# Performance work log

Measured on AMD Instinct MI355X. Metric: run time of the kernel, lower is better.

Reference implementation:

```python
import jax, jax.numpy as jnp
import numpy as np

B, T, N, D, H, M = 2, 12, 325, 64, 8, 3
EPS = 1e-6


def _layer_norm(x, g, b):
    mu = jnp.mean(x, axis=-1, keepdims=True)
    var = jnp.mean(jnp.square(x - mu), axis=-1, keepdims=True)
    return (x - mu) * jax.lax.rsqrt(var + EPS) * g + b


def _meta_w(ste, W1, b1, W2, b2):
    # ste: (b,t,n,d) -> per-token weight matrix (b,t,n,d,d)  [Meta_projection]
    h = jax.nn.relu(jnp.einsum('btnd,de->btne', ste, W1) + b1)
    w = jnp.einsum('btnd,df->btnf', h, W2) + b2
    b_, t_, n_, _ = ste.shape
    return w.reshape(b_, t_, n_, D, D)


def _meta_qkv(q, k, v, ste_q, ste_k, ste_v, mW1, mb1, mW2, mb2):
    wq = _meta_w(ste_q, mW1[0], mb1[0], mW2[0], mb2[0])
    wk = _meta_w(ste_k, mW1[1], mb1[1], mW2[1], mb2[1])
    wv = _meta_w(ste_v, mW1[2], mb1[2], mW2[2], mb2[2])
    mg = lambda x, w: jnp.einsum('btnd,btnde->btne', x, w)  # meta_guide
    return mg(q, wq), mg(k, wk), mg(v, wv)


def _split_heads(x):  # (B,L,d) -> (H*B,L,d/H), head-major = tf.concat(tf.split(x,H,-1),0)
    return jnp.concatenate(jnp.split(x, H, axis=-1), axis=0)


def _concat_heads(x):
    return jnp.concatenate(jnp.split(x, H, axis=0), axis=-1)


def _sdpa(q, k, v, tm=None):
    dk = q.shape[-1]
    scores = jnp.einsum('bqd,bkd->bqk', q, k) / jnp.sqrt(jnp.float32(dk))
    if tm is not None:  # spatial mask (n,n) broadcast over batch*heads
        scores = jnp.where(tm[None] > 0, scores, jnp.float32(-1e9))
    att = jax.nn.softmax(scores, axis=-1)
    return jnp.einsum('bqk,bkd->bqd', att, v)


def _temporal_attn(q, k, v, ste_q, ste_k, ste_v, mW1, mb1, mW2, mb2, Wo):
    b, t, n, d = q.shape
    qg, kg, vg = _meta_qkv(q, k, v, ste_q, ste_k, ste_v, mW1, mb1, mW2, mb2)
    rs = lambda x: x.transpose(0, 2, 1, 3).reshape(b * n, t, d)  # temporal_reshape
    out = _sdpa(_split_heads(rs(qg)), _split_heads(rs(kg)), _split_heads(rs(vg)))
    out = _concat_heads(out).reshape(b, n, t, d).transpose(0, 2, 1, 3)
    return jnp.einsum('btnd,de->btne', out, Wo)


def _spatial_attn(q, k, v, tms, ste_q, ste_k, ste_v, mW1, mb1, mW2, mb2, Wo):
    b, t, n, d = q.shape
    # meta weights are identical across the mask loop in the original -> compute once
    qg, kg, vg = _meta_qkv(q, k, v, ste_q, ste_k, ste_v, mW1, mb1, mW2, mb2)
    rs = lambda x: x.reshape(b * t, n, d)  # spatial_reshape
    q_, k_, v_ = _split_heads(rs(qg)), _split_heads(rs(kg)), _split_heads(rs(vg))
    m = tms.shape[0]
    outs = [_concat_heads(_sdpa(q_, k_, v_, tm=tms[i])) for i in range(m)]
    out = jnp.stack(outs).transpose(1, 2, 3, 0).reshape(b, t, n, d * m)
    return jnp.einsum('btnd,de->btne', out, Wo)


def _ffn(x, W1, W2):
    return jax.nn.relu(x @ W1) @ W2


def setup_inputs() -> dict:
    key = jax.random.key(0)
    ks = jax.random.split(key, 16)
    f = lambda i, shape, s=1.0: jax.random.normal(ks[i], shape, dtype=jnp.float32) * s
    return {
        'queries': f(0, (B, T, N, D)),
        'keys': f(1, (B, T, N, D)),
        'values': f(2, (B, T, N, D)),
        'ste_q': f(3, (B, T, N, D)),
        'ste_k': f(4, (B, T, N, D)),
        'ste_v': f(5, (B, T, N, D)),
        'tms': jax.random.randint(ks[6], (M, N, N), 0, 2, dtype=jnp.int32),
        # 4 attention modules (mta1, msa1, mta2, msa2), 3 meta branches each
        'mW1': f(7, (4, 3, D, D), 0.05),
        'mb1': jnp.zeros((4, 3, D), jnp.float32),
        'mW2': f(8, (4, 3, D, D * D), 0.02),
        'mb2': jnp.zeros((4, 3, D * D), jnp.float32),
        'Wo_t': f(9, (2, D, D), 0.05),          # temporal out-proj (no bias)
        'Wo_s': f(10, (2, M * D, D), 0.05),     # spatial out-proj over d*m (no bias)
        'ffn_W1': f(11, (2, D, D // 4), 0.05),
        'ffn_W2': f(12, (2, D // 4, D), 0.05),
        'ln_gamma': jnp.ones((6, D), jnp.float32),
        'ln_beta': jnp.zeros((6, D), jnp.float32),
    }


def reference(queries, keys, values, ste_q, ste_k, ste_v, tms,
              mW1, mb1, mW2, mb2, Wo_t, Wo_s, ffn_W1, ffn_W2, ln_gamma, ln_beta):
    # Encoderlayer with if_ste=True, if_meta=True, training=False (dropout = identity),
    # b_layers=m_layers=t_layers=1.
    tms_f = tms.astype(jnp.float32)
    x = queries
    # --- begin block: temporal attn + LN, spatial attn + LN ---
    out = _temporal_attn(x, keys, values, ste_q, ste_k, ste_v,
                         mW1[0], mb1[0], mW2[0], mb2[0], Wo_t[0])
    x = _layer_norm(x + out, ln_gamma[0], ln_beta[0])
    out = _spatial_attn(x, x, x, tms_f, ste_q, ste_k, ste_v,
                        mW1[1], mb1[1], mW2[1], mb2[1], Wo_s[0])
    x = _layer_norm(x + out, ln_gamma[1], ln_beta[1])
    # --- medium block: temporal + LN, spatial + LN, FFN + LN ---
    out = _temporal_attn(x, x, x, ste_q, ste_k, ste_v,
                         mW1[2], mb1[2], mW2[2], mb2[2], Wo_t[1])
    x = _layer_norm(x + out, ln_gamma[2], ln_beta[2])
    out = _spatial_attn(x, x, x, tms_f, ste_q, ste_k, ste_v,
                        mW1[3], mb1[3], mW2[3], mb2[3], Wo_s[1])
    x = _layer_norm(x + out, ln_gamma[3], ln_beta[3])
    out = _ffn(x, ffn_W1[0], ffn_W2[0])
    x = _layer_norm(x + out, ln_gamma[4], ln_beta[4])
    # --- end block: FFN + LN ---
    out = _ffn(x, ffn_W1[1], ffn_W2[1])
    x = _layer_norm(x + out, ln_gamma[5], ln_beta[5])
    return x
```

## Files before the change

kernel.cpp:

```cpp
#include <hip/hip_runtime.h>
#include <math.h>

#define BB 2
#define TT 12
#define NN 325
#define DD 64
#define HH 8
#define MM 3
#define NT (BB*TT*NN)
#define NT64 (NT*64)
#define EPS 1e-6f
#define KTOT 4160
#define SEGS 8
#define KPS 41
#define NR 328

typedef _Float16 f16x8 __attribute__((ext_vector_type(8)));
typedef _Float16 f16x2 __attribute__((ext_vector_type(2)));
typedef float f32x4 __attribute__((ext_vector_type(4)));
typedef float f32x2 __attribute__((ext_vector_type(2)));

#if __has_builtin(__builtin_amdgcn_exp2f)
#define EXP2F(x) __builtin_amdgcn_exp2f(x)
#else
#define EXP2F(x) exp2f(x)
#endif

__device__ inline float wave_reduce_sum(float v) {
    #pragma unroll
    for (int o = 32; o > 0; o >>= 1) v += __shfl_xor(v, o, 64);
    return v;
}

__device__ inline float h2f(unsigned u) {
    unsigned short us = (unsigned short)u;
    _Float16 h;
    __builtin_memcpy(&h, &us, 2);
    return (float)h;
}

__global__ __launch_bounds__(256)
void prep_all(const float* __restrict__ mW2, const float* __restrict__ mb2,
              _Float16* __restrict__ Wt,
              const float* __restrict__ mW1, _Float16* __restrict__ W1f,
              const int* __restrict__ tms, unsigned* __restrict__ pmr) {
    const int bx = blockIdx.x;
    const int tid = threadIdx.x;
    if (bx < 780) {
        const int p = bx / 65;
        const int kk0 = (bx % 65) * 64;
        __shared__ float s[64][65];
        #pragma unroll
        for (int pass = 0; pass < 16; ++pass) {
            int idx = pass*256 + tid;
            int kl = idx >> 6, e = idx & 63;
            int kk = kk0 + kl;
            float v = (kk < 4096) ? mW2[(size_t)p*262144 + (size_t)kk*64 + e]
                                  : mb2[(size_t)p*4096 + (size_t)(kk-4096)*64 + e];
            s[kl][e] = v;
        }
        __syncthreads();
        #pragma unroll
        for (int pass = 0; pass < 16; ++pass) {
            int idx = pass*256 + tid;
            int e = idx >> 6, kl = idx & 63;
            Wt[(size_t)p*64*KTOT + (size_t)e*KTOT + kk0 + kl] = (_Float16)s[kl][e];
        }
        return;
    }
    if (bx < 792) {
        const int p = bx - 780;
        #pragma unroll
        for (int i = 0; i < 16; ++i) {
            int idx = i*256 + tid;
            int d = idx >> 6, e = idx & 63;
            W1f[(size_t)p*4096 + e*64 + d] = (_Float16)mW1[(size_t)p*4096 + d*64 + e];
        }
        return;
    }
    int idx = (bx - 792)*256 + tid;
    if (idx >= MM*NN*SEGS) return;
    int seg = idx & 7;
    int nq = (idx >> 3) % NN;
    int i = idx / (SEGS*NN);
    int ks = seg*KPS;
    int ke = (ks + KPS < NN) ? ks + KPS : NN;
    const int* row = tms + ((size_t)i*NN + nq)*NN;
    unsigned w0 = 0, w1 = 0;
    for (int k = ks; k < ke; ++k) {
        int b = k - ks;
        unsigned bit = (row[k] > 0) ? 1u : 0u;
        if (b < 32) w0 |= bit << b; else w1 |= bit << (b - 32);
    }
    pmr[(size_t)idx*2]     = w0;
    pmr[(size_t)idx*2 + 1] = w1;
}

template<int MODE>
__global__ __launch_bounds__(256, 2)
void meta_gemm_t(const float* __restrict__ x0, const float* __restrict__ x1,
                 const float* __restrict__ x2,
                 const float* __restrict__ s0, const float* __restrict__ s1,
                 const float* __restrict__ s2,
                 const _Float16* __restrict__ W1f, const float* __restrict__ b1m,
                 const _Float16* __restrict__ Wtm,
                 void* __restrict__ o0, void* __restrict__ o1, void* __restrict__ o2) {
    const int br = blockIdx.y;
    const int t0 = blockIdx.x * 64;
    const float* xg = (br==0) ? x0 : (br==1) ? x1 : x2;
    const float* sg = (br==0) ? s0 : (br==1) ? s1 : s2;
    const _Float16* W1b = W1f + (size_t)br*4096;
    const float* b1g = b1m + (size_t)br*64;
    const _Float16* W = Wtm + (size_t)br*64*KTOT;
    void* outp = (br==0) ? o0 : (br==1) ? o1 : o2;

    __shared__ _Float16 sx[64*64];
    __shared__ _Float16 ss[64*64];
    __shared__ _Float16 shT[64*68];
    __shared__ _Float16 bB[2][1024*8];

    const int tid = threadIdx.x;
    #pragma unroll
    for (int i = 0; i < 2; ++i) {
        int idx = i*256 + tid;
        int row = idx >> 3, u = idx & 7;
        int t = t0 + row;
        int boff = row*128 + ((u*16) ^ ((row & 7) << 4));
        f16x8 xo, so;
        if (t < NT) {
            const float4* xp = (const float4*)(xg + (size_t)t*64 + u*8);
            float4 a = xp[0], b = xp[1];
            f16x8 xv = {(_Float16)a.x,(_Float16)a.y,(_Float16)a.z,(_Float16)a.w,
                        (_Float16)b.x,(_Float16)b.y,(_Float16)b.z,(_Float16)b.w};
            const float4* sp = (const float4*)(sg + (size_t)t*64 + u*8);
            float4 c = sp[0], d = sp[1];
            f16x8 sv = {(_Float16)c.x,(_Float16)c.y,(_Float16)c.z,(_Float16)c.w,
                        (_Float16)d.x,(_Float16)d.y,(_Float16)d.z,(_Float16)d.w};
            xo = xv; so = sv;
        } else {
            f16x8 z = {(_Float16)0.f,(_Float16)0.f,(_Float16)0.f,(_Float16)0.f,
                       (_Float16)0.f,(_Float16)0.f,(_Float16)0.f,(_Float16)0.f};
            xo = z; so = z;
        }
        *(f16x8*)((char*)sx + boff) = xo;
        *(f16x8*)((char*)ss + boff) = so;
    }
    __syncthreads();

    const int wid = tid >> 6, lane = tid & 63;
    const int col = lane & 15, g = lane >> 4;
    const int wm = wid & 1, wn = wid >> 1;
    const int trow0 = wm*32 + col;
    const int trow1 = trow0 + 16;
    const int rb0 = trow0*128, rb1 = trow1*128;
    const int sz = (trow0 & 7) << 4;

    {
        const int hrow = wid*16 + col;
        const int hrb = hrow*128;
        const int hsz = (hrow & 7) << 4;
        f32x4 ha[4] = {{0,0,0,0},{0,0,0,0},{0,0,0,0},{0,0,0,0}};
        #pragma unroll
        for (int ph = 0; ph < 2; ++ph) {
            int dd = ph*32 + g*8;
            f16x8 sv = *(f16x8*)((char*)ss + hrb + ((dd*2) ^ hsz));
            #pragma unroll
            for (int ni = 0; ni < 4; ++ni) {
                f16x8 bw = *(const f16x8*)(W1b + (size_t)(ni*16+col)*64 + dd);
                ha[ni] = __builtin_amdgcn_mfma_f32_16x16x32_f16(sv, bw, ha[ni], 0, 0, 0);
            }
        }
        #pragma unroll
        for (int ni = 0; ni < 4; ++ni) {
            float bv = b1g[ni*16+col];
            #pragma unroll
            for (int r = 0; r < 4; ++r)
                shT[(wid*16 + g*4 + r)*68 + ni*16 + col] = (_Float16)fmaxf(ha[ni][r] + bv, 0.f);
        }
    }

    f16x8 xv00 = *(f16x8*)((char*)sx + rb0 + (((g*8)*2) ^ sz));
    f16x8 xv01 = *(f16x8*)((char*)sx + rb0 + (((32 + g*8)*2) ^ sz));
    f16x8 xv10 = *(f16x8*)((char*)sx + rb1 + (((g*8)*2) ^ sz));
    f16x8 xv11 = *(f16x8*)((char*)sx + rb1 + (((32 + g*8)*2) ^ sz));

    auto STAGE2 = [&](int bi, int st2) {
        const _Float16* base = W + (size_t)st2*128;
        #pragma unroll
        for (int j = 0; j < 4; ++j) {
            int p = j*256 + tid;
            int t = p >> 9;
            int rest = p & 511;
            int e = rest >> 3, wu = rest & 7;
            const _Float16* src = base + (size_t)t*64 + (size_t)e*KTOT + ((wu ^ (e & 7)) << 3);
            __builtin_amdgcn_global_load_lds(
                (const __attribute__((address_space(1))) void*)src,
                (__attribute__((address_space(3))) void*)&bB[bi][p*8],
                16, 0, 0);
        }
    };
    auto STAGE1 = [&](int bi, int st) {
        const _Float16* base = W + (size_t)st*64;
        #pragma unroll
        for (int j = 0; j < 2; ++j) {
            int p = j*256 + tid;
            int e = p >> 3, wu = p & 7;
            const _Float16* src = base + (size_t)e*KTOT + ((wu ^ (e & 7)) << 3);
            __builtin_amdgcn_global_load_lds(
                (const __attribute__((address_space(1))) void*)src,
                (__attribute__((address_space(3))) void*)&bB[bi][p*8],
                16, 0, 0);
        }
    };

    STAGE2(0, 0);
    STAGE2(1, 1);
    asm volatile("s_waitcnt lgkmcnt(0)" ::: "memory");
    __builtin_amdgcn_sched_barrier(0);

    f32x4 A[2][2] = {{{0,0,0,0},{0,0,0,0}},{{0,0,0,0},{0,0,0,0}}};
    f16x8 hv0 = {}, hv1 = {};

    const int e0 = wn*32 + col;
    const int e1 = e0 + 16;
    const int u00 = e0*8 + (g ^ (e0 & 7));
    const int u01 = e0*8 + ((4 + g) ^ (e0 & 7));
    const int u10 = e1*8 + (g ^ (e1 & 7));
    const int u11 = e1*8 + ((4 + g) ^ (e1 & 7));

    auto COMPUTE = [&](const _Float16* Bb, int ci) {
        #pragma unroll
        for (int t = 0; t < 2; ++t) {
            _Float16 hc0 = hv0[ci*2 + t];
            _Float16 hc1 = hv1[ci*2 + t];
            const _Float16* Bs = Bb + t*512*8;
            f16x8 b00 = *(const f16x8*)((const char*)Bs + u00*16);
            f16x8 b01 = *(const f16x8*)((const char*)Bs + u01*16);
            f16x8 b10 = *(const f16x8*)((const char*)Bs + u10*16);
            f16x8 b11 = *(const f16x8*)((const char*)Bs + u11*16);
            f16x8 p00 = xv00 * hc0;
            f16x8 p10 = xv10 * hc1;
            A[0][0] = __builtin_amdgcn_mfma_f32_16x16x32_f16(p00, b00, A[0][0], 0, 0, 0);
            A[0][1] = __builtin_amdgcn_mfma_f32_16x16x32_f16(p00, b10, A[0][1], 0, 0, 0);
            A[1][0] = __builtin_amdgcn_mfma_f32_16x16x32_f16(p10, b00, A[1][0], 0, 0, 0);
            A[1][1] = __builtin_amdgcn_mfma_f32_16x16x32_f16(p10, b10, A[1][1], 0, 0, 0);
            f16x8 p01 = xv01 * hc0;
            f16x8 p11 = xv11 * hc1;
            A[0][0] = __builtin_amdgcn_mfma_f32_16x16x32_f16(p01, b01, A[0][0], 0, 0, 0);
            A[0][1] = __builtin_amdgcn_mfma_f32_16x16x32_f16(p01, b11, A[0][1], 0, 0, 0);
            A[1][0] = __builtin_amdgcn_mfma_f32_16x16x32_f16(p11, b01, A[1][0], 0, 0, 0);
            A[1][1] = __builtin_amdgcn_mfma_f32_16x16x32_f16(p11, b11, A[1][1], 0, 0, 0);
        }
    };

    for (int q = 0; q < 7; ++q) {
        #pragma unroll
        for (int s = 0; s < 4; ++s) {
            asm volatile("s_waitcnt vmcnt(4)" ::: "memory");
            __builtin_amdgcn_sched_barrier(0);
            __builtin_amdgcn_s_barrier();
            if (s == 0) {
                hv0 = *(f16x8*)&shT[trow0*68 + q*8];
                hv1 = *(f16x8*)&shT[trow1*68 + q*8];
            }
            COMPUTE(bB[s & 1], s);
            __builtin_amdgcn_s_barrier();
            STAGE2(s & 1, 4*q + s + 2);
        }
    }
    asm volatile("s_waitcnt vmcnt(4)" ::: "memory");
    __builtin_amdgcn_sched_barrier(0);
    __builtin_amdgcn_s_barrier();
    hv0 = *(f16x8*)&shT[trow0*68 + 56];
    hv1 = *(f16x8*)&shT[trow1*68 + 56];
    COMPUTE(bB[0], 0);
    __builtin_amdgcn_s_barrier();
    STAGE2(0, 30);

    asm volatile("s_waitcnt vmcnt(4)" ::: "memory");
    __builtin_amdgcn_sched_barrier(0);
    __builtin_amdgcn_s_barrier();
    COMPUTE(bB[1], 1);
    __builtin_amdgcn_s_barrier();
    STAGE2(1, 31);

    asm volatile("s_waitcnt vmcnt(4)" ::: "memory");
    __builtin_amdgcn_sched_barrier(0);
    __builtin_amdgcn_s_barrier();
    COMPUTE(bB[0], 2);
    __builtin_amdgcn_s_barrier();

    asm volatile("s_waitcnt vmcnt(0)" ::: "memory");
    __builtin_amdgcn_sched_barrier(0);
    __builtin_amdgcn_s_barrier();
    COMPUTE(bB[1], 3);
    __builtin_amdgcn_s_barrier();

    STAGE1(0, 64);
    asm volatile("s_waitcnt vmcnt(0)" ::: "memory");
    __builtin_amdgcn_sched_barrier(0);
    __builtin_amdgcn_s_barrier();
    {
        const _Float16* Bs = bB[0];
        f16x8 b00 = *(const f16x8*)((const char*)Bs + u00*16);
        f16x8 b01 = *(const f16x8*)((const char*)Bs + u01*16);
        f16x8 b10 = *(const f16x8*)((const char*)Bs + u10*16);
        f16x8 b11 = *(const f16x8*)((const char*)Bs + u11*16);
        A[0][0] = __builtin_amdgcn_mfma_f32_16x16x32_f16(xv00, b00, A[0][0], 0, 0, 0);
        A[0][1] = __builtin_amdgcn_mfma_f32_16x16x32_f16(xv00, b10, A[0][1], 0, 0, 0);
        A[1][0] = __builtin_amdgcn_mfma_f32_16x16x32_f16(xv10, b00, A[1][0], 0, 0, 0);
        A[1][1] = __builtin_amdgcn_mfma_f32_16x16x32_f16(xv10, b10, A[1][1], 0, 0, 0);
        A[0][0] = __builtin_amdgcn_mfma_f32_16x16x32_f16(xv01, b01, A[0][0], 0, 0, 0);
        A[0][1] = __builtin_amdgcn_mfma_f32_16x16x32_f16(xv01, b11, A[0][1], 0, 0, 0);
        A[1][0] = __builtin_amdgcn_mfma_f32_16x16x32_f16(xv11, b01, A[1][0], 0, 0, 0);
        A[1][1] = __builtin_amdgcn_mfma_f32_16x16x32_f16(xv11, b11, A[1][1], 0, 0, 0);
    }

    if (MODE == 0) {
        float* op = (float*)outp;
        #pragma unroll
        for (int mt = 0; mt < 2; ++mt) {
            #pragma unroll
            for (int nj = 0; nj < 2; ++nj) {
                const int e = e0 + nj*16;
                #pragma unroll
                for (int r = 0; r < 4; ++r) {
                    int t = t0 + wm*32 + mt*16 + g*4 + r;
                    if (t < NT) op[(size_t)t*64 + e] = A[mt][nj][r];
                }
            }
        }
    } else {
        const float KSC = 0.35355339059327373f * 1.4426950408889634f;
        const float scl = (br == 1) ? KSC : 1.f;
        const int bt0 = t0 / NN;
        const int bound = (bt0 + 1)*NN;
        _Float16* op = (_Float16*)outp;
        #pragma unroll
        for (int mt = 0; mt < 2; ++mt) {
            #pragma unroll
            for (int nj = 0; nj < 2; ++nj) {
                const int e = e0 + nj*16;
                const int hh = e >> 3, dd = e & 7;
                #pragma unroll
                for (int r = 0; r < 4; ++r) {
                    int t = t0 + wm*32 + mt*16 + g*4 + r;
                    if (t < NT) {
                        int bt = (t >= bound) ? bt0 + 1 : bt0;
                        int n = t - bt*NN;
                        size_t pidx = ((size_t)(bt*8 + hh)*NR + n)*8 + dd;
                        op[pidx] = (_Float16)(A[mt][nj][r]*scl);
                    }
                }
            }
        }
    }
}

__global__ __launch_bounds__(256)
void temporal_fused(const float* __restrict__ qg, const float* __restrict__ kg,
                    const float* __restrict__ vg, const float* __restrict__ xres,
                    const float* __restrict__ Wo, const float* __restrict__ gamma,
                    const float* __restrict__ beta, float* __restrict__ xout) {
    const int wid = threadIdx.x >> 6, lane = threadIdx.x & 63;
    const int token = blockIdx.x*4 + wid;
    if (token >= NT) return;
    const int n = token % NN;
    const int b = token / (NN*TT);
    const float scale = 0.35355339059327373f;
    const float qv = qg[(size_t)token*64 + lane] * scale;

    float s[TT], v[TT];
    #pragma unroll
    for (int kt = 0; kt < TT; ++kt) {
        size_t base = ((size_t)(b*TT + kt)*NN + n)*64 + lane;
        float kv = kg[base];
        v[kt] = vg[base];
        float d = qv * kv;
        d += __shfl_xor(d, 1, 64);
        d += __shfl_xor(d, 2, 64);
        d += __shfl_xor(d, 4, 64);
        s[kt] = d;
    }
    float m = s[0];
    #pragma unroll
    for (int kt = 1; kt < TT; ++kt) m = fmaxf(m, s[kt]);
    float l = 0.f, O = 0.f;
    #pragma unroll
    for (int kt = 0; kt < TT; ++kt) {
        float p = __expf(s[kt] - m);
        l += p;
        O += p * v[kt];
    }
    O /= l;
    float y0 = 0.f, y1 = 0.f, y2 = 0.f, y3 = 0.f;
    #pragma unroll
    for (int d = 0; d < 64; d += 4) {
        y0 = fmaf(__shfl(O, d,   64), Wo[(d  )*64 + lane], y0);
        y1 = fmaf(__shfl(O, d+1, 64), Wo[(d+1)*64 + lane], y1);
        y2 = fmaf(__shfl(O, d+2, 64), Wo[(d+2)*64 + lane], y2);
        y3 = fmaf(__shfl(O, d+3, 64), Wo[(d+3)*64 + lane], y3);
    }
    float y = (y0 + y1) + (y2 + y3);
    float r = xres[(size_t)token*64 + lane] + y;
    float mu = wave_reduce_sum(r) * (1.f/64.f);
    float diff = r - mu;
    float var = wave_reduce_sum(diff*diff) * (1.f/64.f);
    xout[(size_t)token*64 + lane] = diff * rsqrtf(var + EPS) * gamma[lane] + beta[lane];
}

__global__ __launch_bounds__(256)
void spatial_attn13(const _Float16* __restrict__ Qh, const _Float16* __restrict__ Kh,
                    const _Float16* __restrict__ Vh, const unsigned* __restrict__ pmr,
                    _Float16* __restrict__ outs) {
    const int bh = blockIdx.x;
    const int bt = bh >> 3, h = bh & 7;
    const int q0 = blockIdx.y * 32;
    __shared__ _Float16 KV[NR*16];
    const int tid = threadIdx.x;
    const _Float16* Kb = Kh + (size_t)bh*NR*8;
    const _Float16* Vb = Vh + (size_t)bh*NR*8;

    for (int u = tid; u < NR; u += 256) {
        *(f16x8*)&KV[u*16]     = *(const f16x8*)&Kb[u*8];
        *(f16x8*)&KV[u*16 + 8] = *(const f16x8*)&Vb[u*8];
    }
    __syncthreads();

    const int wid = tid >> 6, lane = tid & 63;
    const int qu = lane >> 3, seg = lane & 7;
    const int nq = q0 + wid*8 + qu;
    const bool act = nq < NN;
    const int qm = act ? nq : NN-1;

    f16x8 qv = *(const f16x8*)(Qh + ((size_t)bh*NR + qm)*8);
    const f16x2* qh2 = (const f16x2*)&qv;
    const int ks = seg*KPS;

    const size_t mbase = ((size_t)qm*SEGS + seg)*2;
    const size_t mstep = (size_t)NN*SEGS*2;
    unsigned w00 = pmr[mbase],           w01 = pmr[mbase+1];
    unsigned w10 = pmr[mstep+mbase],     w11 = pmr[mstep+mbase+1];
    unsigned w20 = pmr[2*mstep+mbase],   w21 = pmr[2*mstep+mbase+1];

    float l0 = 0.f, l1 = 0.f, l2 = 0.f;
    f32x2 O0[4] = {{0,0},{0,0},{0,0},{0,0}};
    f32x2 O1[4] = {{0,0},{0,0},{0,0},{0,0}};
    f32x2 O2[4] = {{0,0},{0,0},{0,0},{0,0}};

    f16x8 kc = *(const f16x8*)&KV[ks*16];
    f16x8 vc = *(const f16x8*)&KV[ks*16 + 8];

    auto step = [&](int j, unsigned b0, unsigned b1, unsigned b2) {
        f16x8 kn = kc, vn = vc;
        if (j + 1 < KPS) {
            kn = *(const f16x8*)&KV[(ks + j + 1)*16];
            vn = *(const f16x8*)&KV[(ks + j + 1)*16 + 8];
        }
        const f16x2* k2 = (const f16x2*)&kc;
        float d = __builtin_amdgcn_fdot2(qh2[0], k2[0], -32.f, false);
        d = __builtin_amdgcn_fdot2(qh2[1], k2[1], d, false);
        d = __builtin_amdgcn_fdot2(qh2[2], k2[2], d, false);
        d = __builtin_amdgcn_fdot2(qh2[3], k2[3], d, false);
        float E = EXP2F(d);
        float E0 = b0 ? E : 0.f;
        float E1 = b1 ? E : 0.f;
        float E2 = b2 ? E : 0.f;
        l0 += E0; l1 += E1; l2 += E2;
        f32x2 e0 = {E0, E0}, e1 = {E1, E1}, e2 = {E2, E2};
        #pragma unroll
        for (int jj = 0; jj < 4; ++jj) {
            f32x2 vp = {(float)vc[2*jj], (float)vc[2*jj+1]};
            O0[jj] += e0 * vp;
            O1[jj] += e1 * vp;
            O2[jj] += e2 * vp;
        }
        kc = kn; vc = vn;
    };
    #pragma unroll
    for (int j = 0; j < 32; ++j)
        step(j, (w00 >> j) & 1u, (w10 >> j) & 1u, (w20 >> j) & 1u);
    #pragma unroll
    for (int j = 32; j < KPS; ++j)
        step(j, (w01 >> (j-32)) & 1u, (w11 >> (j-32)) & 1u, (w21 >> (j-32)) & 1u);

    #pragma unroll
    for (int off = 1; off <= 4; off <<= 1) {
        l0 += __shfl_xor(l0, off, 64);
        l1 += __shfl_xor(l1, off, 64);
        l2 += __shfl_xor(l2, off, 64);
        #pragma unroll
        for (int j = 0; j < 4; ++j) {
            #pragma unroll
            for (int c = 0; c < 2; ++c) {
                O0[j][c] += __shfl_xor(O0[j][c], off, 64);
                O1[j][c] += __shfl_xor(O1[j][c], off, 64);
                O2[j][c] += __shfl_xor(O2[j][c], off, 64);
            }
        }
    }

    if (act && seg == 0) {
        float i0 = 1.f/l0, i1 = 1.f/l1, i2 = 1.f/l2;
        _Float16* op = outs + (size_t)(bt*NN + nq)*192 + h*8;
        f16x8 o0, o1, o2;
        #pragma unroll
        for (int j = 0; j < 4; ++j) {
            o0[2*j] = (_Float16)(O0[j][0]*i0); o0[2*j+1] = (_Float16)(O0[j][1]*i0);
            o1[2*j] = (_Float16)(O1[j][0]*i1); o1[2*j+1] = (_Float16)(O1[j][1]*i1);
            o2[2*j] = (_Float16)(O2[j][0]*i2); o2[2*j+1] = (_Float16)(O2[j][1]*i2);
        }
        *(f16x8*)(op)       = o0;
        *(f16x8*)(op + 64)  = o1;
        *(f16x8*)(op + 128) = o2;
    }
}

__global__ __launch_bounds__(256)
void proj_res_ln_s_kernel(const _Float16* __restrict__ a, const float* __restrict__ xres,
                          const float* __restrict__ Wo, const float* __restrict__ gamma,
                          const float* __restrict__ beta, float* __restrict__ xout) {
    const int wid = threadIdx.x >> 6, lane = threadIdx.x & 63;
    const int token = blockIdx.x*4 + wid;
    if (token >= NT) return;
    const int tu = __builtin_amdgcn_readfirstlane(token);
    const unsigned* aw = (const unsigned*)(a + (size_t)tu*192);
    float y0l = 0.f, y1l = 0.f, y2l = 0.f, y0h = 0.f, y1h = 0.f, y2h = 0.f;
    #pragma unroll
    for (int dd = 0; dd < 32; ++dd) {
        unsigned w0 = aw[dd], w1 = aw[32+dd], w2 = aw[64+dd];
        const float* W0 = Wo + (size_t)(6*dd)*64 + lane;
        y0l = fmaf(h2f(w0 & 0xffffu), W0[0],   y0l);
        y1l = fmaf(h2f(w1 & 0xffffu), W0[64],  y1l);
        y2l = fmaf(h2f(w2 & 0xffffu), W0[128], y2l);
        y0h = fmaf(h2f(w0 >> 16),     W0[192], y0h);
        y1h = fmaf(h2f(w1 >> 16),     W0[256], y1h);
        y2h = fmaf(h2f(w2 >> 16),     W0[320], y2h);
    }
    float y = ((y0l + y0h) + (y1l + y1h)) + (y2l + y2h);
    float r = xres[(size_t)token*64 + lane] + y;
    float mu = wave_reduce_sum(r) * (1.f/64.f);
    float diff = r - mu;
    float var = wave_reduce_sum(diff*diff) * (1.f/64.f);
    xout[(size_t)token*64 + lane] = diff * rsqrtf(var + EPS) * gamma[lane] + beta[lane];
}

__global__ __launch_bounds__(256)
void tail_fused(const _Float16* __restrict__ a, const float* __restrict__ xres,
                const float* __restrict__ Wo,
                const float* __restrict__ W1a, const float* __restrict__ W2a,
                const float* __restrict__ W1b, const float* __restrict__ W2b,
                const float* __restrict__ ln_g, const float* __restrict__ ln_b,
                float* __restrict__ out) {
    const int wid = threadIdx.x >> 6, lane = threadIdx.x & 63;
    const int token = blockIdx.x*4 + wid;
    if (token >= NT) return;
    const int c = lane & 15;

    const int tu = __builtin_amdgcn_readfirstlane(token);
    const unsigned* aw = (const unsigned*)(a + (size_t)tu*192);
    float y0l = 0.f, y1l = 0.f, y2l = 0.f, y0h = 0.f, y1h = 0.f, y2h = 0.f;
    #pragma unroll
    for (int dd = 0; dd < 32; ++dd) {
        unsigned w0 = aw[dd], w1 = aw[32+dd], w2 = aw[64+dd];
        const float* W0 = Wo + (size_t)(6*dd)*64 + lane;
        y0l = fmaf(h2f(w0 & 0xffffu), W0[0],   y0l);
        y1l = fmaf(h2f(w1 & 0xffffu), W0[64],  y1l);
        y2l = fmaf(h2f(w2 & 0xffffu), W0[128], y2l);
        y0h = fmaf(h2f(w0 >> 16),     W0[192], y0h);
        y1h = fmaf(h2f(w1 >> 16),     W0[256], y1h);
        y2h = fmaf(h2f(w2 >> 16),     W0[320], y2h);
    }
    float y = ((y0l + y0h) + (y1l + y1h)) + (y2l + y2h);
    float r = xres[(size_t)token*64 + lane] + y;
    float mu = wave_reduce_sum(r) * (1.f/64.f);
    float diff = r - mu;
    float var = wave_reduce_sum(diff*diff) * (1.f/64.f);
    float x1 = diff * rsqrtf(var + EPS) * ln_g[lane] + ln_b[lane];

    float h0 = 0.f, h1 = 0.f, h2 = 0.f, h3 = 0.f;
    #pragma unroll
    for (int d = 0; d < 64; d += 4) {
        h0 = fmaf(__shfl(x1, d,   64), W1a[(d  )*16 + c], h0);
        h1 = fmaf(__shfl(x1, d+1, 64), W1a[(d+1)*16 + c], h1);
        h2 = fmaf(__shfl(x1, d+2, 64), W1a[(d+2)*16 + c], h2);
        h3 = fmaf(__shfl(x1, d+3, 64), W1a[(d+3)*16 + c], h3);
    }
    float hr = fmaxf((h0 + h1) + (h2 + h3), 0.f);
    float ya = 0.f, yb = 0.f;
    #pragma unroll
    for (int cc = 0; cc < 16; cc += 2) {
        ya = fmaf(__shfl(hr, cc,   64), W2a[(cc  )*64 + lane], ya);
        yb = fmaf(__shfl(hr, cc+1, 64), W2a[(cc+1)*64 + lane], yb);
    }
    r = x1 + (ya + yb);
    mu = wave_reduce_sum(r) * (1.f/64.f);
    diff = r - mu;
    var = wave_reduce_sum(diff*diff) * (1.f/64.f);
    float x2 = diff * rsqrtf(var + EPS) * ln_g[64 + lane] + ln_b[64 + lane];

    h0 = 0.f; h1 = 0.f; h2 = 0.f; h3 = 0.f;
    #pragma unroll
    for (int d = 0; d < 64; d += 4) {
        h0 = fmaf(__shfl(x2, d,   64), W1b[(d  )*16 + c], h0);
        h1 = fmaf(__shfl(x2, d+1, 64), W1b[(d+1)*16 + c], h1);
        h2 = fmaf(__shfl(x2, d+2, 64), W1b[(d+2)*16 + c], h2);
        h3 = fmaf(__shfl(x2, d+3, 64), W1b[(d+3)*16 + c], h3);
    }
    hr = fmaxf((h0 + h1) + (h2 + h3), 0.f);
    ya = 0.f; yb = 0.f;
    #pragma unroll
    for (int cc = 0; cc < 16; cc += 2) {
        ya = fmaf(__shfl(hr, cc,   64), W2b[(cc  )*64 + lane], ya);
        yb = fmaf(__shfl(hr, cc+1, 64), W2b[(cc+1)*64 + lane], yb);
    }
    r = x2 + (ya + yb);
    mu = wave_reduce_sum(r) * (1.f/64.f);
    diff = r - mu;
    var = wave_reduce_sum(diff*diff) * (1.f/64.f);
    out[(size_t)token*64 + lane] = diff * rsqrtf(var + EPS) * ln_g[128 + lane] + ln_b[128 + lane];
}

extern "C" void kernel_launch(void* const* d_in, const int* in_sizes, int n_in,
                              void* d_out, int out_size, void* d_ws, size_t ws_size,
                              hipStream_t stream) {
    const float* queries = (const float*)d_in[0];
    const float* keys    = (const float*)d_in[1];
    const float* values  = (const float*)d_in[2];
    const float* ste_q   = (const float*)d_in[3];
    const float* ste_k   = (const float*)d_in[4];
    const float* ste_v   = (const float*)d_in[5];
    const int*   tms     = (const int*)d_in[6];
    const float* mW1     = (const float*)d_in[7];
    const float* mb1     = (const float*)d_in[8];
    const float* mW2     = (const float*)d_in[9];
    const float* mb2     = (const float*)d_in[10];
    const float* Wo_t    = (const float*)d_in[11];
    const float* Wo_s    = (const float*)d_in[12];
    const float* ffn_W1  = (const float*)d_in[13];
    const float* ffn_W2  = (const float*)d_in[14];
    const float* ln_g    = (const float*)d_in[15];
    const float* ln_b    = (const float*)d_in[16];

    char* p = (char*)d_ws;
    auto carve = [&](size_t bytes) { char* r = p; p += (bytes + 255) & ~(size_t)255; return r; };
    float* xbuf = (float*)carve((size_t)NT64*4);
    float* qg   = (float*)carve((size_t)NT64*4);
    float* kg   = (float*)carve((size_t)NT64*4);
    float* vg   = (float*)carve((size_t)NT64*4);
    _Float16* as_ = (_Float16*)carve((size_t)NT*192*2);
    _Float16* Wt  = (_Float16*)carve((size_t)12*64*KTOT*2);
    _Float16* W1f = (_Float16*)carve((size_t)12*4096*2);
    unsigned* pmr = (unsigned*)carve((size_t)MM*NN*SEGS*2*4);
    _Float16* Qh  = (_Float16*)carve((size_t)BB*TT*HH*NR*8*2);
    _Float16* Kh  = (_Float16*)carve((size_t)BB*TT*HH*NR*8*2);
    _Float16* Vh  = (_Float16*)carve((size_t)BB*TT*HH*NR*8*2);

    const dim3 blk(256);
    const dim3 g_tok(NT/4);
    const dim3 g_sa(BB*TT*HH, 11);
    const dim3 g_gemm((NT + 63)/64, 3);

    prep_all<<<dim3(823), blk, 0, stream>>>(mW2, mb2, Wt, mW1, W1f, tms, pmr);

    meta_gemm_t<0><<<g_gemm, blk, 0, stream>>>(
        queries, keys, values, ste_q, ste_k, ste_v,
        W1f, mb1, Wt, (void*)qg, (void*)kg, (void*)vg);
    temporal_fused<<<g_tok, blk, 0, stream>>>(
        qg, kg, vg, queries, Wo_t, ln_g, ln_b, xbuf);

    meta_gemm_t<1><<<g_gemm, blk, 0, stream>>>(
        xbuf, xbuf, xbuf, ste_q, ste_k, ste_v,
        W1f + (size_t)3*4096, mb1 + (size_t)3*64, Wt + (size_t)3*64*KTOT,
        (void*)Qh, (void*)Kh, (void*)Vh);
    spatial_attn13<<<g_sa, blk, 0, stream>>>(Qh, Kh, Vh, pmr, as_);
    proj_res_ln_s_kernel<<<g_tok, blk, 0, stream>>>(
        as_, xbuf, Wo_s, ln_g + 64, ln_b + 64, xbuf);

    meta_gemm_t<0><<<g_gemm, blk, 0, stream>>>(
        xbuf, xbuf, xbuf, ste_q, ste_k, ste_v,
        W1f + (size_t)6*4096, mb1 + (size_t)6*64, Wt + (size_t)6*64*KTOT,
        (void*)qg, (void*)kg, (void*)vg);
    temporal_fused<<<g_tok, blk, 0, stream>>>(
        qg, kg, vg, xbuf, Wo_t + (size_t)64*64, ln_g + 128, ln_b + 128, xbuf);

    meta_gemm_t<1><<<g_gemm, blk, 0, stream>>>(
        xbuf, xbuf, xbuf, ste_q, ste_k, ste_v,
        W1f + (size_t)9*4096, mb1 + (size_t)9*64, Wt + (size_t)9*64*KTOT,
        (void*)Qh, (void*)Kh, (void*)Vh);
    spatial_attn13<<<g_sa, blk, 0, stream>>>(Qh, Kh, Vh, pmr, as_);
    tail_fused<<<g_tok, blk, 0, stream>>>(
        as_, xbuf, Wo_s + (size_t)192*64,
        ffn_W1, ffn_W2, ffn_W1 + (size_t)64*16, ffn_W2 + (size_t)16*64,
        ln_g + 192, ln_b + 192, (float*)d_out);
}
```

Before: 228.2 us.

## Give each wave a private triple-buffered weight pipeline without block barriers

The block-shared double buffer for the meta-weight tiles is replaced by a per-wave triple buffer, where each wave streams only its own 32-column slice of the weight matrix into LDS. The main K loop becomes a fully unrolled 64-step loop that waits only on its own vmcnt, so the two workgroup barriers per step disappear. The cost is that the two waves sharing a column slice now each load the same weights, doubling global/L2 traffic. LDS use also grows, which may reduce occupancy, and the prefetch depth per step is smaller.

```diff
diff --git a/kernel.cpp b/kernel.cpp
--- a/kernel.cpp
+++ b/kernel.cpp
@@ -117,7 +117,7 @@
     __shared__ _Float16 sx[64*64];
     __shared__ _Float16 ss[64*64];
     __shared__ _Float16 shT[64*68];
-    __shared__ _Float16 bB[2][1024*8];
+    __shared__ _Float16 bW[4][3][256*8];
 
     const int tid = threadIdx.x;
     #pragma unroll
@@ -155,6 +155,23 @@
     const int rb0 = trow0*128, rb1 = trow1*128;
     const int sz = (trow0 & 7) << 4;
 
+    auto STAGE = [&](int slot, int st) {
+        const _Float16* base = W + (size_t)st*64 + (size_t)(wn*32)*KTOT;
+        #pragma unroll
+        for (int j = 0; j < 4; ++j) {
+            int p = j*64 + lane;
+            int el = p >> 3, wu = p & 7;
+            const _Float16* src = base + (size_t)el*KTOT + ((wu ^ (el & 7)) << 3);
+            __builtin_amdgcn_global_load_lds(
+                (const __attribute__((address_space(1))) void*)src,
+                (__attribute__((address_space(3))) void*)&bW[wid][slot][p*8],
+                16, 0, 0);
+        }
+    };
+
+    STAGE(0, 0);
+    STAGE(1, 1);
+
     {
         const int hrow = wid*16 + col;
         const int hrb = hrow*128;
@@ -184,128 +201,56 @@
     f16x8 xv10 = *(f16x8*)((char*)sx + rb1 + (((g*8)*2) ^ sz));
     f16x8 xv11 = *(f16x8*)((char*)sx + rb1 + (((32 + g*8)*2) ^ sz));
 
-    auto STAGE2 = [&](int bi, int st2) {
-        const _Float16* base = W + (size_t)st2*128;
-        #pragma unroll
-        for (int j = 0; j < 4; ++j) {
-            int p = j*256 + tid;
-            int t = p >> 9;
-            int rest = p & 511;
-            int e = rest >> 3, wu = rest & 7;
-            const _Float16* src = base + (size_t)t*64 + (size_t)e*KTOT + ((wu ^ (e & 7)) << 3);
-            __builtin_amdgcn_global_load_lds(
-                (const __attribute__((address_space(1))) void*)src,
-                (__attribute__((address_space(3))) void*)&bB[bi][p*8],
-                16, 0, 0);
-        }
-    };
-    auto STAGE1 = [&](int bi, int st) {
-        const _Float16* base = W + (size_t)st*64;
-        #pragma unroll
-        for (int j = 0; j < 2; ++j) {
-            int p = j*256 + tid;
-            int e = p >> 3, wu = p & 7;
-            const _Float16* src = base + (size_t)e*KTOT + ((wu ^ (e & 7)) << 3);
-            __builtin_amdgcn_global_load_lds(
-                (const __attribute__((address_space(1))) void*)src,
-                (__attribute__((address_space(3))) void*)&bB[bi][p*8],
-                16, 0, 0);
-        }
-    };
-
-    STAGE2(0, 0);
-    STAGE2(1, 1);
     asm volatile("s_waitcnt lgkmcnt(0)" ::: "memory");
     __builtin_amdgcn_sched_barrier(0);
+    __builtin_amdgcn_s_barrier();
 
     f32x4 A[2][2] = {{{0,0,0,0},{0,0,0,0}},{{0,0,0,0},{0,0,0,0}}};
+
+    const int u00 = (col*8      + (g     ^ (col & 7))) * 16;
+    const int u01 = (col*8      + ((4+g) ^ (col & 7))) * 16;
+    const int u10 = ((col+16)*8 + (g     ^ (col & 7))) * 16;
+    const int u11 = ((col+16)*8 + ((4+g) ^ (col & 7))) * 16;
+
+    auto COMPUTE = [&](const _Float16* Bs, _Float16 hc0, _Float16 hc1) {
+        f16x8 b00 = *(const f16x8*)((const char*)Bs + u00);
+        f16x8 b01 = *(const f16x8*)((const char*)Bs + u01);
+        f16x8 b10 = *(const f16x8*)((const char*)Bs + u10);
+        f16x8 b11 = *(const f16x8*)((const char*)Bs + u11);
+        f16x8 p00 = xv00 * hc0;
+        f16x8 p10 = xv10 * hc1;
+        A[0][0] = __builtin_amdgcn_mfma_f32_16x16x32_f16(p00, b00, A[0][0], 0, 0, 0);
+        A[0][1] = __builtin_amdgcn_mfma_f32_16x16x32_f16(p00, b10, A[0][1], 0, 0, 0);
+        A[1][0] = __builtin_amdgcn_mfma_f32_16x16x32_f16(p10, b00, A[1][0], 0, 0, 0);
+        A[1][1] = __builtin_amdgcn_mfma_f32_16x16x32_f16(p10, b10, A[1][1], 0, 0, 0);
+        f16x8 p01 = xv01 * hc0;
+        f16x8 p11 = xv11 * hc1;
+        A[0][0] = __builtin_amdgcn_mfma_f32_16x16x32_f16(p01, b01, A[0][0], 0, 0, 0);
+        A[0][1] = __builtin_amdgcn_mfma_f32_16x16x32_f16(p01, b11, A[0][1], 0, 0, 0);
+        A[1][0] = __builtin_amdgcn_mfma_f32_16x16x32_f16(p11, b01, A[1][0], 0, 0, 0);
+        A[1][1] = __builtin_amdgcn_mfma_f32_16x16x32_f16(p11, b11, A[1][1], 0, 0, 0);
+    };
+
     f16x8 hv0 = {}, hv1 = {};
-
-    const int e0 = wn*32 + col;
-    const int e1 = e0 + 16;
-    const int u00 = e0*8 + (g ^ (e0 & 7));
-    const int u01 = e0*8 + ((4 + g) ^ (e0 & 7));
-    const int u10 = e1*8 + (g ^ (e1 & 7));
-    const int u11 = e1*8 + ((4 + g) ^ (e1 & 7));
-
-    auto COMPUTE = [&](const _Float16* Bb, int ci) {
-        #pragma unroll
-        for (int t = 0; t < 2; ++t) {
-            _Float16 hc0 = hv0[ci*2 + t];
-            _Float16 hc1 = hv1[ci*2 + t];
-            const _Float16* Bs = Bb + t*512*8;
-            f16x8 b00 = *(const f16x8*)((const char*)Bs + u00*16);
-            f16x8 b01 = *(const f16x8*)((const char*)Bs + u01*16);
-            f16x8 b10 = *(const f16x8*)((const char*)Bs + u10*16);
-            f16x8 b11 = *(const f16x8*)((const char*)Bs + u11*16);
-            f16x8 p00 = xv00 * hc0;
-            f16x8 p10 = xv10 * hc1;
-            A[0][0] = __builtin_amdgcn_mfma_f32_16x16x32_f16(p00, b00, A[0][0], 0, 0, 0);
-            A[0][1] = __builtin_amdgcn_mfma_f32_16x16x32_f16(p00, b10, A[0][1], 0, 0, 0);
-            A[1][0] = __builtin_amdgcn_mfma_f32_16x16x32_f16(p10, b00, A[1][0], 0, 0, 0);
-            A[1][1] = __builtin_amdgcn_mfma_f32_16x16x32_f16(p10, b10, A[1][1], 0, 0, 0);
-            f16x8 p01 = xv01 * hc0;
-            f16x8 p11 = xv11 * hc1;
-            A[0][0] = __builtin_amdgcn_mfma_f32_16x16x32_f16(p01, b01, A[0][0], 0, 0, 0);
-            A[0][1] = __builtin_amdgcn_mfma_f32_16x16x32_f16(p01, b11, A[0][1], 0, 0, 0);
-            A[1][0] = __builtin_amdgcn_mfma_f32_16x16x32_f16(p11, b01, A[1][0], 0, 0, 0);
-            A[1][1] = __builtin_amdgcn_mfma_f32_16x16x32_f16(p11, b11, A[1][1], 0, 0, 0);
-        }
-    };
-
-    for (int q = 0; q < 7; ++q) {
-        #pragma unroll
-        for (int s = 0; s < 4; ++s) {
-            asm volatile("s_waitcnt vmcnt(4)" ::: "memory");
-            __builtin_amdgcn_sched_barrier(0);
-            __builtin_amdgcn_s_barrier();
-            if (s == 0) {
-                hv0 = *(f16x8*)&shT[trow0*68 + q*8];
-                hv1 = *(f16x8*)&shT[trow1*68 + q*8];
-            }
-            COMPUTE(bB[s & 1], s);
-            __builtin_amdgcn_s_barrier();
-            STAGE2(s & 1, 4*q + s + 2);
-        }
-    }
-    asm volatile("s_waitcnt vmcnt(4)" ::: "memory");
-    __builtin_amdgcn_sched_barrier(0);
-    __builtin_amdgcn_s_barrier();
-    hv0 = *(f16x8*)&shT[trow0*68 + 56];
-    hv1 = *(f16x8*)&shT[trow1*68 + 56];
-    COMPUTE(bB[0], 0);
-    __builtin_amdgcn_s_barrier();
-    STAGE2(0, 30);
-
-    asm volatile("s_waitcnt vmcnt(4)" ::: "memory");
-    __builtin_amdgcn_sched_barrier(0);
-    __builtin_amdgcn_s_barrier();
-    COMPUTE(bB[1], 1);
-    __builtin_amdgcn_s_barrier();
-    STAGE2(1, 31);
-
-    asm volatile("s_waitcnt vmcnt(4)" ::: "memory");
-    __builtin_amdgcn_sched_barrier(0);
-    __builtin_amdgcn_s_barrier();
-    COMPUTE(bB[0], 2);
-    __builtin_amdgcn_s_barrier();
-
+    #pragma unroll
+    for (int i = 0; i < 64; ++i) {
+        if ((i & 7) == 0) {
+            hv0 = *(f16x8*)&shT[trow0*68 + i];
+            hv1 = *(f16x8*)&shT[trow1*68 + i];
+        }
+        asm volatile("s_waitcnt vmcnt(4)" ::: "memory");
+        __builtin_amdgcn_sched_barrier(0);
+        COMPUTE(&bW[wid][i % 3][0], hv0[i & 7], hv1[i & 7]);
+        if (i < 63) STAGE((i + 2) % 3, i + 2);
+    }
     asm volatile("s_waitcnt vmcnt(0)" ::: "memory");
     __builtin_amdgcn_sched_barrier(0);
-    __builtin_amdgcn_s_barrier();
-    COMPUTE(bB[1], 3);
-    __builtin_amdgcn_s_barrier();
-
-    STAGE1(0, 64);
-    asm volatile("s_waitcnt vmcnt(0)" ::: "memory");
-    __builtin_amdgcn_sched_barrier(0);
-    __builtin_amdgcn_s_barrier();
     {
-        const _Float16* Bs = bB[0];
-        f16x8 b00 = *(const f16x8*)((const char*)Bs + u00*16);
-        f16x8 b01 = *(const f16x8*)((const char*)Bs + u01*16);
-        f16x8 b10 = *(const f16x8*)((const char*)Bs + u10*16);
-        f16x8 b11 = *(const f16x8*)((const char*)Bs + u11*16);
+        const _Float16* Bs = &bW[wid][1][0];
+        f16x8 b00 = *(const f16x8*)((const char*)Bs + u00);
+        f16x8 b01 = *(const f16x8*)((const char*)Bs + u01);
+        f16x8 b10 = *(const f16x8*)((const char*)Bs + u10);
+        f16x8 b11 = *(const f16x8*)((const char*)Bs + u11);
         A[0][0] = __builtin_amdgcn_mfma_f32_16x16x32_f16(xv00, b00, A[0][0], 0, 0, 0);
         A[0][1] = __builtin_amdgcn_mfma_f32_16x16x32_f16(xv00, b10, A[0][1], 0, 0, 0);
         A[1][0] = __builtin_amdgcn_mfma_f32_16x16x32_f16(xv10, b00, A[1][0], 0, 0, 0);
@@ -316,6 +261,7 @@
         A[1][1] = __builtin_amdgcn_mfma_f32_16x16x32_f16(xv11, b11, A[1][1], 0, 0, 0);
     }
 
+    const int e0 = wn*32 + col;
     if (MODE == 0) {
         float* op = (float*)outp;
         #pragma unroll
```

Measured after the change: 244.2 us. 1.07x slower.
